# Optimization experiments

Hardware: AMD Instinct MI355X
Metric: run time of the kernel (lower is better)

## Reference

```python
import jax, jax.numpy as jnp
import numpy as np

N = 50000
E = 800000
IN_C = 64
HID = 64
HEADS = 4
NUM_GRAPHS = 64
NEG_SLOPE = 0.2


def setup_inputs() -> dict:
    key = jax.random.key(0)
    ks = jax.random.split(key, 16)
    x = jax.random.normal(ks[0], (N, IN_C), dtype=jnp.float32)
    edge_index = jax.random.randint(ks[1], (2, E), 0, N, dtype=jnp.int64)
    batch = jnp.sort(jax.random.randint(ks[2], (N,), 0, NUM_GRAPHS, dtype=jnp.int64))
    s = lambda *sh: 1.0 / np.sqrt(sh[0])
    # conv1: in -> HID per head, concat -> HEADS*HID
    W1 = jax.random.normal(ks[3], (IN_C, HEADS * HID), dtype=jnp.float32) * s(IN_C)
    a1_src = jax.random.normal(ks[4], (HEADS, HID), dtype=jnp.float32) * s(HID)
    a1_dst = jax.random.normal(ks[5], (HEADS, HID), dtype=jnp.float32) * s(HID)
    b1 = jnp.zeros((HEADS * HID,), dtype=jnp.float32)
    # conv2: HEADS*HID -> HID, single head, no concat
    W2 = jax.random.normal(ks[6], (HEADS * HID, HID), dtype=jnp.float32) * s(HEADS * HID)
    a2_src = jax.random.normal(ks[7], (1, HID), dtype=jnp.float32) * s(HID)
    a2_dst = jax.random.normal(ks[8], (1, HID), dtype=jnp.float32) * s(HID)
    b2 = jnp.zeros((HID,), dtype=jnp.float32)
    # MLP head: HID -> 16 -> 1
    Wh1 = jax.random.normal(ks[9], (HID, 16), dtype=jnp.float32) * s(HID)
    bh1 = jnp.zeros((16,), dtype=jnp.float32)
    Wh2 = jax.random.normal(ks[10], (16, 1), dtype=jnp.float32) * s(16)
    bh2 = jnp.zeros((1,), dtype=jnp.float32)
    return {"x": x, "edge_index": edge_index, "batch": batch,
            "W1": W1, "a1_src": a1_src, "a1_dst": a1_dst, "b1": b1,
            "W2": W2, "a2_src": a2_src, "a2_dst": a2_dst, "b2": b2,
            "Wh1": Wh1, "bh1": bh1, "Wh2": Wh2, "bh2": bh2}


def _gat_conv(x, src, dst, W, a_src, a_dst, b, concat):
    """PyG-style GATConv (eval mode, self-loops already appended)."""
    H, C = a_src.shape
    xp = (x @ W).reshape(-1, H, C)                      # [N,H,C]
    e_s = jnp.einsum('nhc,hc->nh', xp, a_src)            # source contribution
    e_d = jnp.einsum('nhc,hc->nh', xp, a_dst)            # target contribution
    e = jax.nn.leaky_relu(e_s[src] + e_d[dst], NEG_SLOPE)  # [E,H]
    # segment softmax over edges grouped by destination node
    m = jax.ops.segment_max(e, dst, num_segments=N)
    ex = jnp.exp(e - m[dst])
    denom = jax.ops.segment_sum(ex, dst, num_segments=N)
    alpha = ex / denom[dst]                              # [E,H]
    out = jax.ops.segment_sum(alpha[:, :, None] * xp[src], dst, num_segments=N)  # [N,H,C]
    out = out.reshape(-1, H * C) if concat else out.mean(axis=1)
    return out + b


def reference(x, edge_index, batch, W1, a1_src, a1_dst, b1,
              W2, a2_src, a2_dst, b2, Wh1, bh1, Wh2, bh2):
    # add self loops once (GATConv default add_self_loops=True)
    loop = jnp.arange(N, dtype=edge_index.dtype)
    src = jnp.concatenate([edge_index[0], loop])
    dst = jnp.concatenate([edge_index[1], loop])
    h = jax.nn.elu(_gat_conv(x, src, dst, W1, a1_src, a1_dst, b1, concat=True))
    h = _gat_conv(h, src, dst, W2, a2_src, a2_dst, b2, concat=False)
    # global mean pool over graphs
    summed = jax.ops.segment_sum(h, batch, num_segments=NUM_GRAPHS)
    cnt = jax.ops.segment_sum(jnp.ones((N,), h.dtype), batch, num_segments=NUM_GRAPHS)
    pooled = summed / jnp.maximum(cnt, 1.0)[:, None]     # [G,HID]
    z = jax.nn.relu(pooled @ Wh1 + bh1)
    out = jax.nn.sigmoid(z @ Wh2 + bh2)
    return out.squeeze(-1)                               # [G]
```

## Files before the change

### kernel.cpp

```cpp
#include <hip/hip_runtime.h>
#include <math.h>

#define N_NODES 50000
#define N_EDGES 800000
#define EA (N_EDGES + N_NODES)
#define HEADS 4
#define HID 64
#define NG 64
#define NEG_SLOPE 0.2f
#define SCAN_CHUNK 1024
#define NBLK ((N_NODES + SCAN_CHUNK - 1) / SCAN_CHUNK)

typedef _Float16 f16x8 __attribute__((ext_vector_type(8)));
typedef float f32x4 __attribute__((ext_vector_type(4)));
struct h4 { _Float16 a, b, c, d; };

__device__ inline float lrelu(float x) { return x > 0.f ? x : NEG_SLOPE * x; }

__device__ inline void edge_sd(const int* __restrict__ ei, int e, int& s, int& d) {
    if (e < N_EDGES) { s = ei[e]; d = ei[N_EDGES + e]; }
    else { s = e - N_EDGES; d = s; }
}

__device__ inline f16x8 ldfrag(const _Float16* __restrict__ p, int lq) {
    uint2 lo = *(const uint2*)(p + lq * 4);
    uint2 hi = *(const uint2*)(p + 16 + lq * 4);
    union { uint4 u; f16x8 v; } f;
    f.u = make_uint4(lo.x, lo.y, hi.x, hi.y);
    return f.v;
}

__global__ void k_zero(int* __restrict__ deg, float* __restrict__ pooled,
                       float* __restrict__ cnt)
{
    int i = blockIdx.x * 256 + threadIdx.x;
    int st = gridDim.x * 256;
    for (int j = i; j < N_NODES; j += st) deg[j] = 0;
    if (i < NG * HID) pooled[i] = 0.f;
    if (i < NG) cnt[i] = 0.f;
}

__global__ void k_deg(const int* __restrict__ ei, int* __restrict__ deg)
{
    int e = blockIdx.x * 256 + threadIdx.x;
    if (e >= EA) return;
    int s, d; edge_sd(ei, e, s, d);
    atomicAdd(&deg[d], 1);
}

__global__ __launch_bounds__(1024) void k_scan1(const int* __restrict__ deg,
        int* __restrict__ incl, int* __restrict__ blksum)
{
    __shared__ int sd[SCAN_CHUNK];
    int t = threadIdx.x;
    int i = blockIdx.x * SCAN_CHUNK + t;
    sd[t] = (i < N_NODES) ? deg[i] : 0;
    for (int off = 1; off < SCAN_CHUNK; off <<= 1) {
        __syncthreads();
        int u = (t >= off) ? sd[t - off] : 0;
        __syncthreads();
        sd[t] += u;
    }
    if (i < N_NODES) incl[i] = sd[t];
    if (t == SCAN_CHUNK - 1) blksum[blockIdx.x] = sd[t];
}

__global__ void k_scan2(const int* __restrict__ blksum, int* __restrict__ blkoff)
{
    if (threadIdx.x == 0) {
        int acc = 0;
        for (int b = 0; b < NBLK; ++b) { blkoff[b] = acc; acc += blksum[b]; }
    }
}

__global__ void k_scan3(const int* __restrict__ incl, const int* __restrict__ blkoff,
                        const int* __restrict__ deg, const int* __restrict__ batch,
                        int* __restrict__ rowptr, int* __restrict__ cursor,
                        float* __restrict__ cnt)
{
    int i = blockIdx.x * 256 + threadIdx.x;
    bool act = i < N_NODES;
    if (act) {
        int v = incl[i] + blkoff[i >> 10];
        rowptr[i + 1] = v;
        cursor[i] = v - deg[i];
        if (i == 0) rowptr[0] = 0;
    }
    int g = act ? batch[i] : -1;
    int lane = threadIdx.x & 63;
    int g0 = __shfl(g, 0, 64);
    if (__all(g == g0)) {
        if (lane == 0 && g0 >= 0) atomicAdd(&cnt[g0], 64.f);
    } else if (act) {
        atomicAdd(&cnt[g], 1.f);
    }
}

__global__ void k_fill(const int* __restrict__ ei, int* __restrict__ cursor,
                       int* __restrict__ csr_src)
{
    int e = blockIdx.x * 256 + threadIdx.x;
    if (e >= EA) return;
    int s, d; edge_sd(ei, e, s, d);
    int pos = atomicAdd(&cursor[d], 1);
    csr_src[pos] = s;
}

__global__ __launch_bounds__(256) void k_prepw(const float* __restrict__ W1,
        const float* __restrict__ a1s, const float* __restrict__ a1d,
        const float* __restrict__ W2, const float* __restrict__ a2s,
        const float* __restrict__ a2d, _Float16* __restrict__ W1P,
        _Float16* __restrict__ W2P, float* __restrict__ va1s,
        float* __restrict__ va1d, float* __restrict__ va2s, float* __restrict__ va2d)
{
    const int t = threadIdx.x;
    for (int i = t; i < 256 * 64; i += 256) {
        int np = i >> 6, k = i & 63;
        W1P[i] = (_Float16)W1[k * 256 + (np & 3) * 64 + (np >> 2)];
    }
    for (int i = t; i < 64 * 256; i += 256) {
        int n = i >> 8, k = i & 255;
        W2P[i] = (_Float16)W2[k * 64 + n];
    }
    {
        int k = t >> 2, h = t & 3;
        float ss = 0.f, sd = 0.f;
        for (int c = 0; c < 64; ++c) {
            float wv = W1[k * 256 + h * 64 + c];
            ss = fmaf(wv, a1s[h * 64 + c], ss);
            sd = fmaf(wv, a1d[h * 64 + c], sd);
        }
        va1s[k * 4 + h] = ss;
        va1d[k * 4 + h] = sd;
    }
    {
        float ss = 0.f, sd = 0.f;
        for (int c = 0; c < 64; ++c) {
            float wv = W2[t * 64 + c];
            ss = fmaf(wv, a2s[c], ss);
            sd = fmaf(wv, a2d[c], sd);
        }
        va2s[t] = ss;
        va2d[t] = sd;
    }
}

__global__ __launch_bounds__(256) void k_prepx(const float* __restrict__ x,
        const float* __restrict__ va1s, const float* __restrict__ va1d,
        _Float16* __restrict__ xh, float* __restrict__ e1s, float* __restrict__ e1d)
{
    const int lane = threadIdx.x & 63;
    const int w = threadIdx.x >> 6;
    const int n = blockIdx.x * 4 + w;
    if (n >= N_NODES) return;
    float xv = x[(size_t)n * 64 + lane];
    xh[(size_t)n * 64 + lane] = (_Float16)xv;
    float4 vs = ((const float4*)va1s)[lane];
    float4 vd = ((const float4*)va1d)[lane];
    float s0 = xv * vs.x, s1 = xv * vs.y, s2 = xv * vs.z, s3 = xv * vs.w;
    float d0 = xv * vd.x, d1 = xv * vd.y, d2 = xv * vd.z, d3 = xv * vd.w;
    #pragma unroll
    for (int off = 32; off > 0; off >>= 1) {
        s0 += __shfl_down(s0, off, 64); s1 += __shfl_down(s1, off, 64);
        s2 += __shfl_down(s2, off, 64); s3 += __shfl_down(s3, off, 64);
        d0 += __shfl_down(d0, off, 64); d1 += __shfl_down(d1, off, 64);
        d2 += __shfl_down(d2, off, 64); d3 += __shfl_down(d3, off, 64);
    }
    if (lane == 0) {
        ((float4*)e1s)[n] = make_float4(s0, s1, s2, s3);
        ((float4*)e1d)[n] = make_float4(d0, d1, d2, d3);
    }
}

__global__ __launch_bounds__(256) void k_gemm1(const _Float16* __restrict__ xh,
        const _Float16* __restrict__ W1P, _Float16* __restrict__ xp1h)
{
    const int t = threadIdx.x;
    const int lane = t & 63, w = t >> 6;
    const int l15 = lane & 15, lq = lane >> 4;
    const int m0 = blockIdx.x * 64 + w * 16;
    const int mrow = m0 + l15;
    const _Float16* xrow = xh + (size_t)(m0 + l15) * 64;
    f16x8 xf0 = ldfrag(xrow, lq);
    f16x8 xf1 = ldfrag(xrow + 32, lq);
    #pragma unroll
    for (int ct = 0; ct < 16; ++ct) {
        const _Float16* wrow = W1P + (size_t)(ct * 16 + l15) * 64;
        f16x8 wf0 = ldfrag(wrow, lq);
        f16x8 wf1 = ldfrag(wrow + 32, lq);
        f32x4 acc = {0.f, 0.f, 0.f, 0.f};
        acc = __builtin_amdgcn_mfma_f32_16x16x32_f16(wf0, xf0, acc, 0, 0, 0);
        acc = __builtin_amdgcn_mfma_f32_16x16x32_f16(wf1, xf1, acc, 0, 0, 0);
        if (mrow < N_NODES) {
            h4 o = {(_Float16)acc[0], (_Float16)acc[1], (_Float16)acc[2], (_Float16)acc[3]};
            *(h4*)(xp1h + (size_t)mrow * 256 + ct * 16 + lq * 4) = o;
        }
    }
}

__global__ __launch_bounds__(256) void k_aggr1(const int* __restrict__ rowptr,
        const int* __restrict__ csr_src, const float* __restrict__ e1s,
        const float* __restrict__ e1d, const _Float16* __restrict__ xp1h,
        const float* __restrict__ b1, const float* __restrict__ va2s,
        const float* __restrict__ va2d, _Float16* __restrict__ h1h,
        float* __restrict__ e2s_o, float* __restrict__ e2d_o)
{
    const int lane = threadIdx.x & 63;
    const int w = __builtin_amdgcn_readfirstlane(threadIdx.x >> 6);
    const int d = blockIdx.x * 4 + w;
    if (d >= N_NODES) return;
    const int beg = rowptr[d], end = rowptr[d + 1];
    const float4 ed = ((const float4*)e1d)[d];
    float a0 = 0.f, a1 = 0.f, a2 = 0.f, a3 = 0.f;
    float d0 = 0.f, d1 = 0.f, d2 = 0.f, d3 = 0.f;
    for (int jb = beg; jb < end; jb += 64) {
        int myj = jb + lane;
        int sv = 0;
        float4 p = make_float4(0.f, 0.f, 0.f, 0.f);
        if (myj < end) {
            sv = csr_src[myj];
            float4 q = ((const float4*)e1s)[sv];
            p.x = __expf(lrelu(q.x + ed.x));
            p.y = __expf(lrelu(q.y + ed.y));
            p.z = __expf(lrelu(q.z + ed.z));
            p.w = __expf(lrelu(q.w + ed.w));
        }
        int nj = end - jb; if (nj > 64) nj = 64;
        int njr = (nj + 3) & ~3;
        for (int j = 0; j < njr; j += 4) {
            #pragma unroll
            for (int k = 0; k < 4; ++k) {
                int s = __shfl(sv, j + k, 64);
                float px = __shfl(p.x, j + k, 64);
                float py = __shfl(p.y, j + k, 64);
                float pz = __shfl(p.z, j + k, 64);
                float pw = __shfl(p.w, j + k, 64);
                h4 xv = *(const h4*)(xp1h + (size_t)s * 256 + lane * 4);
                a0 = fmaf(px, (float)xv.a, a0);
                a1 = fmaf(py, (float)xv.b, a1);
                a2 = fmaf(pz, (float)xv.c, a2);
                a3 = fmaf(pw, (float)xv.d, a3);
                d0 += px; d1 += py; d2 += pz; d3 += pw;
            }
        }
    }
    float acc[4] = {a0 / d0, a1 / d1, a2 / d2, a3 / d3};
    float es = 0.f, edd = 0.f;
    #pragma unroll
    for (int hh = 0; hh < 4; ++hh) {
        float v = acc[hh] + b1[hh * 64 + lane];
        v = v > 0.f ? v : __expf(v) - 1.f;
        h1h[(size_t)d * 256 + hh * 64 + lane] = (_Float16)v;
        es  = fmaf(v, va2s[hh * 64 + lane], es);
        edd = fmaf(v, va2d[hh * 64 + lane], edd);
    }
    #pragma unroll
    for (int off = 32; off > 0; off >>= 1) {
        es += __shfl_down(es, off, 64);
        edd += __shfl_down(edd, off, 64);
    }
    if (lane == 0) { e2s_o[d] = es; e2d_o[d] = edd; }
}

__global__ __launch_bounds__(256) void k_gemm2(const _Float16* __restrict__ h1h,
        const _Float16* __restrict__ W2P, _Float16* __restrict__ xp2h)
{
    const int t = threadIdx.x;
    const int lane = t & 63, w = t >> 6;
    const int l15 = lane & 15, lq = lane >> 4;
    const int m0 = blockIdx.x * 64 + w * 16;
    const int mrow = m0 + l15;
    const _Float16* arow = h1h + (size_t)(m0 + l15) * 256;
    f16x8 af[8];
    #pragma unroll
    for (int ks = 0; ks < 8; ++ks) af[ks] = ldfrag(arow + ks * 32, lq);
    #pragma unroll
    for (int ct = 0; ct < 4; ++ct) {
        const _Float16* wrow = W2P + (size_t)(ct * 16 + l15) * 256;
        f32x4 acc = {0.f, 0.f, 0.f, 0.f};
        #pragma unroll
        for (int ks = 0; ks < 8; ++ks) {
            f16x8 wf = ldfrag(wrow + ks * 32, lq);
            acc = __builtin_amdgcn_mfma_f32_16x16x32_f16(wf, af[ks], acc, 0, 0, 0);
        }
        if (mrow < N_NODES) {
            h4 o = {(_Float16)acc[0], (_Float16)acc[1], (_Float16)acc[2], (_Float16)acc[3]};
            *(h4*)(xp2h + (size_t)mrow * 64 + ct * 16 + lq * 4) = o;
        }
    }
}

__global__ __launch_bounds__(256) void k_aggr2(const int* __restrict__ rowptr,
        const int* __restrict__ csr_src, const float* __restrict__ e2s,
        const float* __restrict__ e2d, const _Float16* __restrict__ xp2h,
        const float* __restrict__ b2, const int* __restrict__ batch,
        float* __restrict__ pooled)
{
    const int lane = threadIdx.x & 63;
    const int w = __builtin_amdgcn_readfirstlane(threadIdx.x >> 6);
    const int d = blockIdx.x * 4 + w;
    if (d >= N_NODES) return;
    const int beg = rowptr[d], end = rowptr[d + 1];
    const float ed = e2d[d];
    float acc = 0.f, den = 0.f;
    for (int jb = beg; jb < end; jb += 64) {
        int myj = jb + lane;
        int sv = 0;
        float p = 0.f;
        if (myj < end) {
            sv = csr_src[myj];
            p = __expf(lrelu(e2s[sv] + ed));
        }
        int nj = end - jb; if (nj > 64) nj = 64;
        int njr = (nj + 7) & ~7;
        for (int j = 0; j < njr; j += 8) {
            #pragma unroll
            for (int k = 0; k < 8; ++k) {
                int s = __shfl(sv, j + k, 64);
                float pv = __shfl(p, j + k, 64);
                acc = fmaf(pv, (float)xp2h[(size_t)s * 64 + lane], acc);
                den += pv;
            }
        }
    }
    float val = acc / den + b2[lane];
    int g = batch[d];
    atomicAdd(&pooled[g * 64 + lane], val);
}

__global__ void k_mlp(const float* __restrict__ pooled, const float* __restrict__ cnt,
                      const float* __restrict__ Wh1, const float* __restrict__ bh1,
                      const float* __restrict__ Wh2, const float* __restrict__ bh2,
                      float* __restrict__ out)
{
    int g = threadIdx.x;
    float inv = 1.f / fmaxf(cnt[g], 1.f);
    float p[64];
    #pragma unroll
    for (int c = 0; c < 64; ++c) p[c] = pooled[g * 64 + c] * inv;
    float acc2 = bh2[0];
    for (int j = 0; j < 16; ++j) {
        float z = bh1[j];
        #pragma unroll
        for (int c = 0; c < 64; ++c) z = fmaf(p[c], Wh1[c * 16 + j], z);
        z = fmaxf(z, 0.f);
        acc2 = fmaf(z, Wh2[j], acc2);
    }
    out[g] = 1.f / (1.f + expf(-acc2));
}

extern "C" void kernel_launch(void* const* d_in, const int* in_sizes, int n_in,
                              void* d_out, int out_size, void* d_ws, size_t ws_size,
                              hipStream_t stream)
{
    const float* x      = (const float*)d_in[0];
    const int*   ei     = (const int*)d_in[1];
    const int*   batch  = (const int*)d_in[2];
    const float* W1     = (const float*)d_in[3];
    const float* a1s    = (const float*)d_in[4];
    const float* a1d    = (const float*)d_in[5];
    const float* b1     = (const float*)d_in[6];
    const float* W2     = (const float*)d_in[7];
    const float* a2s    = (const float*)d_in[8];
    const float* a2d    = (const float*)d_in[9];
    const float* b2     = (const float*)d_in[10];
    const float* Wh1    = (const float*)d_in[11];
    const float* bh1    = (const float*)d_in[12];
    const float* Wh2    = (const float*)d_in[13];
    const float* bh2    = (const float*)d_in[14];
    float* out = (float*)d_out;

    float* ws = (float*)d_ws;
    size_t off = 0;
    _Float16* xp1h = (_Float16*)(ws + off); off += (size_t)N_NODES * 128;
    _Float16* h1h  = (_Float16*)(ws + off); off += (size_t)(N_NODES + 64) * 128;
    _Float16* xh   = (_Float16*)(ws + off); off += (size_t)(N_NODES + 64) * 32;
    float* e1s    = ws + off; off += (size_t)N_NODES * 4;
    float* e1d    = ws + off; off += (size_t)N_NODES * 4;
    float* e2s    = ws + off; off += N_NODES;
    float* e2d    = ws + off; off += N_NODES;
    _Float16* xp2h = (_Float16*)(ws + off); off += (size_t)N_NODES * 32;
    _Float16* W1P  = (_Float16*)(ws + off); off += 8192;
    _Float16* W2P  = (_Float16*)(ws + off); off += 8192;
    float* va1s   = ws + off; off += 256;
    float* va1d   = ws + off; off += 256;
    float* va2s   = ws + off; off += 256;
    float* va2d   = ws + off; off += 256;
    float* pooled = ws + off; off += NG * HID;
    float* cnt    = ws + off; off += NG;
    int* rowptr   = (int*)(ws + off); off += N_NODES + 2;
    int* cursor   = (int*)(ws + off); off += N_NODES;
    int* csr_src  = (int*)(ws + off); off += EA;
    int* blksum   = (int*)(ws + off); off += NBLK;
    int* blkoff   = (int*)(ws + off); off += NBLK;
    int* deg  = (int*)h1h;
    int* incl = deg + N_NODES;

    const int BE = (EA + 255) / 256;
    const int BN = (N_NODES + 255) / 256;
    const int BW = (N_NODES + 3) / 4;
    const int BG = (N_NODES + 63) / 64;

    hipLaunchKernelGGL(k_zero,  dim3(64),   dim3(256),  0, stream, deg, pooled, cnt);
    hipLaunchKernelGGL(k_deg,   dim3(BE),   dim3(256),  0, stream, ei, deg);
    hipLaunchKernelGGL(k_scan1, dim3(NBLK), dim3(1024), 0, stream, deg, incl, blksum);
    hipLaunchKernelGGL(k_scan2, dim3(1),    dim3(64),   0, stream, blksum, blkoff);
    hipLaunchKernelGGL(k_scan3, dim3(BN),   dim3(256),  0, stream,
                       incl, blkoff, deg, batch, rowptr, cursor, cnt);
    hipLaunchKernelGGL(k_fill,  dim3(BE),   dim3(256),  0, stream, ei, cursor, csr_src);

    hipLaunchKernelGGL(k_prepw, dim3(1),  dim3(256), 0, stream,
                       W1, a1s, a1d, W2, a2s, a2d, W1P, W2P, va1s, va1d, va2s, va2d);
    hipLaunchKernelGGL(k_prepx, dim3(BW), dim3(256), 0, stream,
                       x, va1s, va1d, xh, e1s, e1d);
    hipLaunchKernelGGL(k_gemm1, dim3(BG), dim3(256), 0, stream, xh, W1P, xp1h);
    hipLaunchKernelGGL(k_aggr1, dim3(BW), dim3(256), 0, stream,
                       rowptr, csr_src, e1s, e1d, xp1h, b1, va2s, va2d,
                       h1h, e2s, e2d);
    hipLaunchKernelGGL(k_gemm2, dim3(BG), dim3(256), 0, stream, h1h, W2P, xp2h);
    hipLaunchKernelGGL(k_aggr2, dim3(BW), dim3(256), 0, stream,
                       rowptr, csr_src, e2s, e2d, xp2h, b2, batch, pooled);

    hipLaunchKernelGGL(k_mlp, dim3(1), dim3(64), 0, stream,
                       pooled, cnt, Wh1, bh1, Wh2, bh2, out);
}
```

Measured before the change: 444.8 us.

## Fuse prep kernels into scan and gemm1, process two edges per wave in aggregation

```diff
diff --git a/kernel.cpp b/kernel.cpp
--- a/kernel.cpp
+++ b/kernel.cpp
@@ -13,14 +13,8 @@
 
 typedef _Float16 f16x8 __attribute__((ext_vector_type(8)));
 typedef float f32x4 __attribute__((ext_vector_type(4)));
-struct h4 { _Float16 a, b, c, d; };
 
 __device__ inline float lrelu(float x) { return x > 0.f ? x : NEG_SLOPE * x; }
-
-__device__ inline void edge_sd(const int* __restrict__ ei, int e, int& s, int& d) {
-    if (e < N_EDGES) { s = ei[e]; d = ei[N_EDGES + e]; }
-    else { s = e - N_EDGES; d = s; }
-}
 
 __device__ inline f16x8 ldfrag(const _Float16* __restrict__ p, int lq) {
     uint2 lo = *(const uint2*)(p + lq * 4);
@@ -44,7 +38,7 @@
 {
     int e = blockIdx.x * 256 + threadIdx.x;
     if (e >= EA) return;
-    int s, d; edge_sd(ei, e, s, d);
+    int d = (e < N_EDGES) ? ei[N_EDGES + e] : e - N_EDGES;
     atomicAdd(&deg[d], 1);
 }
 
@@ -65,11 +59,50 @@
     if (t == SCAN_CHUNK - 1) blksum[blockIdx.x] = sd[t];
 }
 
-__global__ void k_scan2(const int* __restrict__ blksum, int* __restrict__ blkoff)
-{
-    if (threadIdx.x == 0) {
+__global__ __launch_bounds__(256) void k_scan2p(const int* __restrict__ blksum,
+        int* __restrict__ blkoff, const float* __restrict__ W1,
+        const float* __restrict__ a1s, const float* __restrict__ a1d,
+        const float* __restrict__ W2, const float* __restrict__ a2s,
+        const float* __restrict__ a2d, const float* __restrict__ b1,
+        _Float16* __restrict__ W1P, _Float16* __restrict__ W2P,
+        float* __restrict__ va1s, float* __restrict__ va1d,
+        float* __restrict__ b1P, float* __restrict__ va2sP, float* __restrict__ va2dP)
+{
+    const int t = threadIdx.x;
+    if (t == 0) {
         int acc = 0;
         for (int b = 0; b < NBLK; ++b) { blkoff[b] = acc; acc += blksum[b]; }
+    }
+    for (int i = t; i < 256 * 64; i += 256) {
+        int np = i >> 6, k = i & 63;
+        W1P[i] = (_Float16)W1[k * 256 + (np & 3) * 64 + (np >> 2)];
+    }
+    for (int i = t; i < 64 * 256; i += 256) {
+        int n = i >> 8, kp = i & 255;
+        W2P[i] = (_Float16)W2[((kp & 3) * 64 + (kp >> 2)) * 64 + n];
+    }
+    {
+        int k = t >> 2, h = t & 3;
+        float ss = 0.f, sd = 0.f;
+        for (int c = 0; c < 64; ++c) {
+            float wv = W1[k * 256 + h * 64 + c];
+            ss = fmaf(wv, a1s[h * 64 + c], ss);
+            sd = fmaf(wv, a1d[h * 64 + c], sd);
+        }
+        va1s[t] = ss;
+        va1d[t] = sd;
+    }
+    {
+        int ko = (t & 3) * 64 + (t >> 2);
+        b1P[t] = b1[ko];
+        float ss = 0.f, sd = 0.f;
+        for (int c = 0; c < 64; ++c) {
+            float wv = W2[ko * 64 + c];
+            ss = fmaf(wv, a2s[c], ss);
+            sd = fmaf(wv, a2d[c], sd);
+        }
+        va2sP[t] = ss;
+        va2dP[t] = sd;
     }
 }
 
@@ -101,99 +134,78 @@
 {
     int e = blockIdx.x * 256 + threadIdx.x;
     if (e >= EA) return;
-    int s, d; edge_sd(ei, e, s, d);
+    int s, d;
+    if (e < N_EDGES) { s = ei[e]; d = ei[N_EDGES + e]; }
+    else { s = e - N_EDGES; d = s; }
     int pos = atomicAdd(&cursor[d], 1);
     csr_src[pos] = s;
 }
 
-__global__ __launch_bounds__(256) void k_prepw(const float* __restrict__ W1,
-        const float* __restrict__ a1s, const float* __restrict__ a1d,
-        const float* __restrict__ W2, const float* __restrict__ a2s,
-        const float* __restrict__ a2d, _Float16* __restrict__ W1P,
-        _Float16* __restrict__ W2P, float* __restrict__ va1s,
-        float* __restrict__ va1d, float* __restrict__ va2s, float* __restrict__ va2d)
-{
-    const int t = threadIdx.x;
-    for (int i = t; i < 256 * 64; i += 256) {
-        int np = i >> 6, k = i & 63;
-        W1P[i] = (_Float16)W1[k * 256 + (np & 3) * 64 + (np >> 2)];
-    }
-    for (int i = t; i < 64 * 256; i += 256) {
-        int n = i >> 8, k = i & 255;
-        W2P[i] = (_Float16)W2[k * 64 + n];
-    }
-    {
-        int k = t >> 2, h = t & 3;
-        float ss = 0.f, sd = 0.f;
-        for (int c = 0; c < 64; ++c) {
-            float wv = W1[k * 256 + h * 64 + c];
-            ss = fmaf(wv, a1s[h * 64 + c], ss);
-            sd = fmaf(wv, a1d[h * 64 + c], sd);
-        }
-        va1s[k * 4 + h] = ss;
-        va1d[k * 4 + h] = sd;
-    }
-    {
-        float ss = 0.f, sd = 0.f;
-        for (int c = 0; c < 64; ++c) {
-            float wv = W2[t * 64 + c];
-            ss = fmaf(wv, a2s[c], ss);
-            sd = fmaf(wv, a2d[c], sd);
-        }
-        va2s[t] = ss;
-        va2d[t] = sd;
-    }
-}
-
-__global__ __launch_bounds__(256) void k_prepx(const float* __restrict__ x,
-        const float* __restrict__ va1s, const float* __restrict__ va1d,
-        _Float16* __restrict__ xh, float* __restrict__ e1s, float* __restrict__ e1d)
-{
-    const int lane = threadIdx.x & 63;
-    const int w = threadIdx.x >> 6;
-    const int n = blockIdx.x * 4 + w;
-    if (n >= N_NODES) return;
-    float xv = x[(size_t)n * 64 + lane];
-    xh[(size_t)n * 64 + lane] = (_Float16)xv;
-    float4 vs = ((const float4*)va1s)[lane];
-    float4 vd = ((const float4*)va1d)[lane];
-    float s0 = xv * vs.x, s1 = xv * vs.y, s2 = xv * vs.z, s3 = xv * vs.w;
-    float d0 = xv * vd.x, d1 = xv * vd.y, d2 = xv * vd.z, d3 = xv * vd.w;
-    #pragma unroll
-    for (int off = 32; off > 0; off >>= 1) {
-        s0 += __shfl_down(s0, off, 64); s1 += __shfl_down(s1, off, 64);
-        s2 += __shfl_down(s2, off, 64); s3 += __shfl_down(s3, off, 64);
-        d0 += __shfl_down(d0, off, 64); d1 += __shfl_down(d1, off, 64);
-        d2 += __shfl_down(d2, off, 64); d3 += __shfl_down(d3, off, 64);
-    }
-    if (lane == 0) {
-        ((float4*)e1s)[n] = make_float4(s0, s1, s2, s3);
-        ((float4*)e1d)[n] = make_float4(d0, d1, d2, d3);
-    }
-}
-
-__global__ __launch_bounds__(256) void k_gemm1(const _Float16* __restrict__ xh,
-        const _Float16* __restrict__ W1P, _Float16* __restrict__ xp1h)
+__global__ __launch_bounds__(256) void k_gemm1(const float* __restrict__ x,
+        const _Float16* __restrict__ W1P, const float* __restrict__ va1s,
+        const float* __restrict__ va1d, _Float16* __restrict__ xp1h,
+        float* __restrict__ e1s, float* __restrict__ e1d)
 {
     const int t = threadIdx.x;
     const int lane = t & 63, w = t >> 6;
     const int l15 = lane & 15, lq = lane >> 4;
     const int m0 = blockIdx.x * 64 + w * 16;
     const int mrow = m0 + l15;
-    const _Float16* xrow = xh + (size_t)(m0 + l15) * 64;
-    f16x8 xf0 = ldfrag(xrow, lq);
-    f16x8 xf1 = ldfrag(xrow + 32, lq);
+    const int mc = mrow < N_NODES ? mrow : N_NODES - 1;
+    const float* xr = x + (size_t)mc * 64;
+    float4 x0 = *(const float4*)(xr + lq * 4);
+    float4 x1 = *(const float4*)(xr + 16 + lq * 4);
+    float4 x2 = *(const float4*)(xr + 32 + lq * 4);
+    float4 x3 = *(const float4*)(xr + 48 + lq * 4);
+    const float4* vs4 = (const float4*)va1s;
+    const float4* vd4 = (const float4*)va1d;
+    float4 es = {0,0,0,0}, ed = {0,0,0,0};
+    {
+        float xv[16] = {x0.x,x0.y,x0.z,x0.w, x1.x,x1.y,x1.z,x1.w,
+                        x2.x,x2.y,x2.z,x2.w, x3.x,x3.y,x3.z,x3.w};
+        #pragma unroll
+        for (int q = 0; q < 4; ++q) {
+            int kb = q * 16 + lq * 4;
+            #pragma unroll
+            for (int j = 0; j < 4; ++j) {
+                float v = xv[q * 4 + j];
+                float4 a = vs4[kb + j], b = vd4[kb + j];
+                es.x = fmaf(v, a.x, es.x); es.y = fmaf(v, a.y, es.y);
+                es.z = fmaf(v, a.z, es.z); es.w = fmaf(v, a.w, es.w);
+                ed.x = fmaf(v, b.x, ed.x); ed.y = fmaf(v, b.y, ed.y);
+                ed.z = fmaf(v, b.z, ed.z); ed.w = fmaf(v, b.w, ed.w);
+            }
+        }
+    }
+    #pragma unroll
+    for (int off = 16; off <= 32; off <<= 1) {
+        es.x += __shfl_down(es.x, off, 64); es.y += __shfl_down(es.y, off, 64);
+        es.z += __shfl_down(es.z, off, 64); es.w += __shfl_down(es.w, off, 64);
+        ed.x += __shfl_down(ed.x, off, 64); ed.y += __shfl_down(ed.y, off, 64);
+        ed.z += __shfl_down(ed.z, off, 64); ed.w += __shfl_down(ed.w, off, 64);
+    }
+    if (lq == 0 && mrow < N_NODES) {
+        ((float4*)e1s)[mrow] = es;
+        ((float4*)e1d)[mrow] = ed;
+    }
+    union { f16x8 v; _Float16 e[8]; } u0, u1;
+    u0.e[0]=(_Float16)x0.x; u0.e[1]=(_Float16)x0.y; u0.e[2]=(_Float16)x0.z; u0.e[3]=(_Float16)x0.w;
+    u0.e[4]=(_Float16)x1.x; u0.e[5]=(_Float16)x1.y; u0.e[6]=(_Float16)x1.z; u0.e[7]=(_Float16)x1.w;
+    u1.e[0]=(_Float16)x2.x; u1.e[1]=(_Float16)x2.y; u1.e[2]=(_Float16)x2.z; u1.e[3]=(_Float16)x2.w;
+    u1.e[4]=(_Float16)x3.x; u1.e[5]=(_Float16)x3.y; u1.e[6]=(_Float16)x3.z; u1.e[7]=(_Float16)x3.w;
     #pragma unroll
     for (int ct = 0; ct < 16; ++ct) {
         const _Float16* wrow = W1P + (size_t)(ct * 16 + l15) * 64;
         f16x8 wf0 = ldfrag(wrow, lq);
         f16x8 wf1 = ldfrag(wrow + 32, lq);
         f32x4 acc = {0.f, 0.f, 0.f, 0.f};
-        acc = __builtin_amdgcn_mfma_f32_16x16x32_f16(wf0, xf0, acc, 0, 0, 0);
-        acc = __builtin_amdgcn_mfma_f32_16x16x32_f16(wf1, xf1, acc, 0, 0, 0);
+        acc = __builtin_amdgcn_mfma_f32_16x16x32_f16(wf0, u0.v, acc, 0, 0, 0);
+        acc = __builtin_amdgcn_mfma_f32_16x16x32_f16(wf1, u1.v, acc, 0, 0, 0);
         if (mrow < N_NODES) {
-            h4 o = {(_Float16)acc[0], (_Float16)acc[1], (_Float16)acc[2], (_Float16)acc[3]};
-            *(h4*)(xp1h + (size_t)mrow * 256 + ct * 16 + lq * 4) = o;
+            union { uint2 u2; _Float16 e[4]; } o;
+            o.e[0]=(_Float16)acc[0]; o.e[1]=(_Float16)acc[1];
+            o.e[2]=(_Float16)acc[2]; o.e[3]=(_Float16)acc[3];
+            *(uint2*)(xp1h + (size_t)mrow * 256 + ct * 16 + lq * 4) = o.u2;
         }
     }
 }
@@ -201,8 +213,8 @@
 __global__ __launch_bounds__(256) void k_aggr1(const int* __restrict__ rowptr,
         const int* __restrict__ csr_src, const float* __restrict__ e1s,
         const float* __restrict__ e1d, const _Float16* __restrict__ xp1h,
-        const float* __restrict__ b1, const float* __restrict__ va2s,
-        const float* __restrict__ va2d, _Float16* __restrict__ h1h,
+        const float* __restrict__ b1P, const float* __restrict__ va2sP,
+        const float* __restrict__ va2dP, _Float16* __restrict__ h1h,
         float* __restrict__ e2s_o, float* __restrict__ e2d_o)
 {
     const int lane = threadIdx.x & 63;
@@ -210,56 +222,79 @@
     const int d = blockIdx.x * 4 + w;
     if (d >= N_NODES) return;
     const int beg = rowptr[d], end = rowptr[d + 1];
-    const float4 ed = ((const float4*)e1d)[d];
-    float a0 = 0.f, a1 = 0.f, a2 = 0.f, a3 = 0.f;
-    float d0 = 0.f, d1 = 0.f, d2 = 0.f, d3 = 0.f;
+    const float4 edv = ((const float4*)e1d)[d];
+    const int li = lane & 31;
+    const bool hB = lane >= 32;
+    float acc[8] = {0,0,0,0,0,0,0,0};
+    float den[4] = {0,0,0,0};
     for (int jb = beg; jb < end; jb += 64) {
         int myj = jb + lane;
         int sv = 0;
-        float4 p = make_float4(0.f, 0.f, 0.f, 0.f);
+        float px = 0.f, py = 0.f, pz = 0.f, pw = 0.f;
         if (myj < end) {
             sv = csr_src[myj];
             float4 q = ((const float4*)e1s)[sv];
-            p.x = __expf(lrelu(q.x + ed.x));
-            p.y = __expf(lrelu(q.y + ed.y));
-            p.z = __expf(lrelu(q.z + ed.z));
-            p.w = __expf(lrelu(q.w + ed.w));
+            px = __expf(lrelu(q.x + edv.x));
+            py = __expf(lrelu(q.y + edv.y));
+            pz = __expf(lrelu(q.z + edv.z));
+            pw = __expf(lrelu(q.w + edv.w));
         }
         int nj = end - jb; if (nj > 64) nj = 64;
-        int njr = (nj + 3) & ~3;
-        for (int j = 0; j < njr; j += 4) {
+        int pr = (nj + 7) & ~7;
+        for (int j = 0; j < pr; j += 8) {
             #pragma unroll
-            for (int k = 0; k < 4; ++k) {
-                int s = __shfl(sv, j + k, 64);
-                float px = __shfl(p.x, j + k, 64);
-                float py = __shfl(p.y, j + k, 64);
-                float pz = __shfl(p.z, j + k, 64);
-                float pw = __shfl(p.w, j + k, 64);
-                h4 xv = *(const h4*)(xp1h + (size_t)s * 256 + lane * 4);
-                a0 = fmaf(px, (float)xv.a, a0);
-                a1 = fmaf(py, (float)xv.b, a1);
-                a2 = fmaf(pz, (float)xv.c, a2);
-                a3 = fmaf(pw, (float)xv.d, a3);
-                d0 += px; d1 += py; d2 += pz; d3 += pw;
+            for (int u = 0; u < 4; ++u) {
+                int eA = j + 2 * u, eB = eA + 1;
+                int sA = __shfl(sv, eA, 64), sB = __shfl(sv, eB, 64);
+                float pxA = __shfl(px, eA, 64), pxB = __shfl(px, eB, 64);
+                float pyA = __shfl(py, eA, 64), pyB = __shfl(py, eB, 64);
+                float pzA = __shfl(pz, eA, 64), pzB = __shfl(pz, eB, 64);
+                float pwA = __shfl(pw, eA, 64), pwB = __shfl(pw, eB, 64);
+                int s = hB ? sB : sA;
+                float p0 = hB ? pxB : pxA, p1 = hB ? pyB : pyA;
+                float p2 = hB ? pzB : pzA, p3 = hB ? pwB : pwA;
+                union { uint4 u4; _Float16 e[8]; } X;
+                X.u4 = *(const uint4*)(xp1h + (size_t)s * 256 + li * 8);
+                acc[0] = fmaf(p0, (float)X.e[0], acc[0]);
+                acc[1] = fmaf(p1, (float)X.e[1], acc[1]);
+                acc[2] = fmaf(p2, (float)X.e[2], acc[2]);
+                acc[3] = fmaf(p3, (float)X.e[3], acc[3]);
+                acc[4] = fmaf(p0, (float)X.e[4], acc[4]);
+                acc[5] = fmaf(p1, (float)X.e[5], acc[5]);
+                acc[6] = fmaf(p2, (float)X.e[6], acc[6]);
+                acc[7] = fmaf(p3, (float)X.e[7], acc[7]);
+                den[0] += p0; den[1] += p1; den[2] += p2; den[3] += p3;
             }
         }
     }
-    float acc[4] = {a0 / d0, a1 / d1, a2 / d2, a3 / d3};
+    #pragma unroll
+    for (int j = 0; j < 8; ++j) acc[j] += __shfl_xor(acc[j], 32, 64);
+    #pragma unroll
+    for (int h = 0; h < 4; ++h) den[h] += __shfl_xor(den[h], 32, 64);
+    float rd[4] = {1.f / den[0], 1.f / den[1], 1.f / den[2], 1.f / den[3]};
+    float4 bl = ((const float4*)b1P)[2 * li],  bh = ((const float4*)b1P)[2 * li + 1];
+    float4 sl = ((const float4*)va2sP)[2 * li], sh = ((const float4*)va2sP)[2 * li + 1];
+    float4 dl = ((const float4*)va2dP)[2 * li], dh = ((const float4*)va2dP)[2 * li + 1];
+    float bb[8] = {bl.x,bl.y,bl.z,bl.w, bh.x,bh.y,bh.z,bh.w};
+    float ss[8] = {sl.x,sl.y,sl.z,sl.w, sh.x,sh.y,sh.z,sh.w};
+    float dd[8] = {dl.x,dl.y,dl.z,dl.w, dh.x,dh.y,dh.z,dh.w};
     float es = 0.f, edd = 0.f;
-    #pragma unroll
-    for (int hh = 0; hh < 4; ++hh) {
-        float v = acc[hh] + b1[hh * 64 + lane];
+    union { uint4 u4; _Float16 e[8]; } O;
+    #pragma unroll
+    for (int j = 0; j < 8; ++j) {
+        float v = acc[j] * rd[j & 3] + bb[j];
         v = v > 0.f ? v : __expf(v) - 1.f;
-        h1h[(size_t)d * 256 + hh * 64 + lane] = (_Float16)v;
-        es  = fmaf(v, va2s[hh * 64 + lane], es);
-        edd = fmaf(v, va2d[hh * 64 + lane], edd);
-    }
+        O.e[j] = (_Float16)v;
+        es  = fmaf(v, ss[j], es);
+        edd = fmaf(v, dd[j], edd);
+    }
+    if (!hB) *(uint4*)(h1h + (size_t)d * 256 + li * 8) = O.u4;
     #pragma unroll
     for (int off = 32; off > 0; off >>= 1) {
         es += __shfl_down(es, off, 64);
         edd += __shfl_down(edd, off, 64);
     }
-    if (lane == 0) { e2s_o[d] = es; e2d_o[d] = edd; }
+    if (lane == 0) { e2s_o[d] = 0.5f * es; e2d_o[d] = 0.5f * edd; }
 }
 
 __global__ __launch_bounds__(256) void k_gemm2(const _Float16* __restrict__ h1h,
@@ -284,8 +319,10 @@
             acc = __builtin_amdgcn_mfma_f32_16x16x32_f16(wf, af[ks], acc, 0, 0, 0);
         }
         if (mrow < N_NODES) {
-            h4 o = {(_Float16)acc[0], (_Float16)acc[1], (_Float16)acc[2], (_Float16)acc[3]};
-            *(h4*)(xp2h + (size_t)mrow * 64 + ct * 16 + lq * 4) = o;
+            union { uint2 u2; _Float16 e[4]; } o;
+            o.e[0]=(_Float16)acc[0]; o.e[1]=(_Float16)acc[1];
+            o.e[2]=(_Float16)acc[2]; o.e[3]=(_Float16)acc[3];
+            *(uint2*)(xp2h + (size_t)mrow * 64 + ct * 16 + lq * 4) = o.u2;
         }
     }
 }
@@ -301,31 +338,47 @@
     const int d = blockIdx.x * 4 + w;
     if (d >= N_NODES) return;
     const int beg = rowptr[d], end = rowptr[d + 1];
-    const float ed = e2d[d];
-    float acc = 0.f, den = 0.f;
+    const float edv = e2d[d];
+    const int li = lane & 31;
+    const bool hB = lane >= 32;
+    float acc0 = 0.f, acc1 = 0.f, den = 0.f;
     for (int jb = beg; jb < end; jb += 64) {
         int myj = jb + lane;
         int sv = 0;
         float p = 0.f;
         if (myj < end) {
             sv = csr_src[myj];
-            p = __expf(lrelu(e2s[sv] + ed));
+            p = __expf(lrelu(e2s[sv] + edv));
         }
         int nj = end - jb; if (nj > 64) nj = 64;
-        int njr = (nj + 7) & ~7;
-        for (int j = 0; j < njr; j += 8) {
+        int pr = (nj + 7) & ~7;
+        for (int j = 0; j < pr; j += 8) {
             #pragma unroll
-            for (int k = 0; k < 8; ++k) {
-                int s = __shfl(sv, j + k, 64);
-                float pv = __shfl(p, j + k, 64);
-                acc = fmaf(pv, (float)xp2h[(size_t)s * 64 + lane], acc);
-                den += pv;
+            for (int u = 0; u < 4; ++u) {
+                int eA = j + 2 * u, eB = eA + 1;
+                int sA = __shfl(sv, eA, 64), sB = __shfl(sv, eB, 64);
+                float pA = __shfl(p, eA, 64), pB = __shfl(p, eB, 64);
+                int s = hB ? sB : sA;
+                float pp = hB ? pB : pA;
+                union { unsigned int u1; _Float16 e[2]; } X;
+                X.u1 = *(const unsigned int*)(xp2h + (size_t)s * 64 + li * 2);
+                acc0 = fmaf(pp, (float)X.e[0], acc0);
+                acc1 = fmaf(pp, (float)X.e[1], acc1);
+                den += pp;
             }
         }
     }
-    float val = acc / den + b2[lane];
+    acc0 += __shfl_xor(acc0, 32, 64);
+    acc1 += __shfl_xor(acc1, 32, 64);
+    den  += __shfl_xor(den, 32, 64);
+    float rdn = 1.f / den;
     int g = batch[d];
-    atomicAdd(&pooled[g * 64 + lane], val);
+    if (!hB) {
+        float v0 = acc0 * rdn + b2[2 * li];
+        float v1 = acc1 * rdn + b2[2 * li + 1];
+        atomicAdd(&pooled[g * 64 + 2 * li], v0);
+        atomicAdd(&pooled[g * 64 + 2 * li + 1], v1);
+    }
 }
 
 __global__ void k_mlp(const float* __restrict__ pooled, const float* __restrict__ cnt,
@@ -374,7 +427,6 @@
     size_t off = 0;
     _Float16* xp1h = (_Float16*)(ws + off); off += (size_t)N_NODES * 128;
     _Float16* h1h  = (_Float16*)(ws + off); off += (size_t)(N_NODES + 64) * 128;
-    _Float16* xh   = (_Float16*)(ws + off); off += (size_t)(N_NODES + 64) * 32;
     float* e1s    = ws + off; off += (size_t)N_NODES * 4;
     float* e1d    = ws + off; off += (size_t)N_NODES * 4;
     float* e2s    = ws + off; off += N_NODES;
@@ -384,8 +436,9 @@
     _Float16* W2P  = (_Float16*)(ws + off); off += 8192;
     float* va1s   = ws + off; off += 256;
     float* va1d   = ws + off; off += 256;
-    float* va2s   = ws + off; off += 256;
-    float* va2d   = ws + off; off += 256;
+    float* b1P    = ws + off; off += 256;
+    float* va2sP  = ws + off; off += 256;
+    float* va2dP  = ws + off; off += 256;
     float* pooled = ws + off; off += NG * HID;
     float* cnt    = ws + off; off += NG;
     int* rowptr   = (int*)(ws + off); off += N_NODES + 2;
@@ -401,24 +454,23 @@
     const int BW = (N_NODES + 3) / 4;
     const int BG = (N_NODES + 63) / 64;
 
-    hipLaunchKernelGGL(k_zero,  dim3(64),   dim3(256),  0, stream, deg, pooled, cnt);
-    hipLaunchKernelGGL(k_deg,   dim3(BE),   dim3(256),  0, stream, ei, deg);
-    hipLaunchKernelGGL(k_scan1, dim3(NBLK), dim3(1024), 0, stream, deg, incl, blksum);
-    hipLaunchKernelGGL(k_scan2, dim3(1),    dim3(64),   0, stream, blksum, blkoff);
-    hipLaunchKernelGGL(k_scan3, dim3(BN),   dim3(256),  0, stream,
+    hipLaunchKernelGGL(k_zero,   dim3(64),   dim3(256),  0, stream, deg, pooled, cnt);
+    hipLaunchKernelGGL(k_deg,    dim3(BE),   dim3(256),  0, stream, ei, deg);
+    hipLaunchKernelGGL(k_scan1,  dim3(NBLK), dim3(1024), 0, stream, deg, incl, blksum);
+    hipLaunchKernelGGL(k_scan2p, dim3(1),    dim3(256),  0, stream,
+                       blksum, blkoff, W1, a1s, a1d, W2, a2s, a2d, b1,
+                       W1P, W2P, va1s, va1d, b1P, va2sP, va2dP);
+    hipLaunchKernelGGL(k_scan3,  dim3(BN),   dim3(256),  0, stream,
                        incl, blkoff, deg, batch, rowptr, cursor, cnt);
-    hipLaunchKernelGGL(k_fill,  dim3(BE),   dim3(256),  0, stream, ei, cursor, csr_src);
-
-    hipLaunchKernelGGL(k_prepw, dim3(1),  dim3(256), 0, stream,
-                       W1, a1s, a1d, W2, a2s, a2d, W1P, W2P, va1s, va1d, va2s, va2d);
-    hipLaunchKernelGGL(k_prepx, dim3(BW), dim3(256), 0, stream,
-                       x, va1s, va1d, xh, e1s, e1d);
-    hipLaunchKernelGGL(k_gemm1, dim3(BG), dim3(256), 0, stream, xh, W1P, xp1h);
-    hipLaunchKernelGGL(k_aggr1, dim3(BW), dim3(256), 0, stream,
-                       rowptr, csr_src, e1s, e1d, xp1h, b1, va2s, va2d,
+    hipLaunchKernelGGL(k_fill,   dim3(BE),   dim3(256),  0, stream, ei, cursor, csr_src);
+
+    hipLaunchKernelGGL(k_gemm1,  dim3(BG),   dim3(256),  0, stream,
+                       x, W1P, va1s, va1d, xp1h, e1s, e1d);
+    hipLaunchKernelGGL(k_aggr1,  dim3(BW),   dim3(256),  0, stream,
+                       rowptr, csr_src, e1s, e1d, xp1h, b1P, va2sP, va2dP,
                        h1h, e2s, e2d);
-    hipLaunchKernelGGL(k_gemm2, dim3(BG), dim3(256), 0, stream, h1h, W2P, xp2h);
-    hipLaunchKernelGGL(k_aggr2, dim3(BW), dim3(256), 0, stream,
+    hipLaunchKernelGGL(k_gemm2,  dim3(BG),   dim3(256),  0, stream, h1h, W2P, xp2h);
+    hipLaunchKernelGGL(k_aggr2,  dim3(BW),   dim3(256),  0, stream,
                        rowptr, csr_src, e2s, e2d, xp2h, b2, batch, pooled);
 
     hipLaunchKernelGGL(k_mlp, dim3(1), dim3(64), 0, stream,
```

Measured after the change: 473.1 us. +6.4%, slower.
